# Kernel optimization log

Measured on AMD Instinct MI355X. Metric: run time of the kernel, lower is better.

Reference implementation:

```python
import jax, jax.numpy as jnp
import numpy as np

NB, NA, NC, NH, NW = 64, 5, 20, 64, 64
MAX_BBOX = 50
ANCHORS = jnp.array([[1.3221, 1.73145], [3.19275, 4.00944], [5.05587, 8.09892],
                     [9.47112, 4.84053], [11.2364, 10.0071]], dtype=jnp.float32)
COORD_SCALE = 1.0
NOOBJ_SCALE = 1.0
OBJ_SCALE = 1.0
CLASS_SCALE = 1.0
SIL_THRESH = 0.6


def iou_xywh(b1, b2):
    # center-format IoU, matching marvis bbox_ious(x1y1x2y2=False)
    x1, y1, w1, h1 = b1[..., 0], b1[..., 1], b1[..., 2], b1[..., 3]
    x2, y2, w2, h2 = b2[..., 0], b2[..., 1], b2[..., 2], b2[..., 3]
    Mx = jnp.maximum(x1 + w1 * 0.5, x2 + w2 * 0.5)
    mx = jnp.minimum(x1 - w1 * 0.5, x2 - w2 * 0.5)
    My = jnp.maximum(y1 + h1 * 0.5, y2 + h2 * 0.5)
    my = jnp.minimum(y1 - h1 * 0.5, y2 - h2 * 0.5)
    cw = w1 + w2 - (Mx - mx)
    ch = h1 + h2 - (My - my)
    carea = jnp.where((cw <= 0) | (ch <= 0), 0.0, cw * ch)
    uarea = w1 * h1 + w2 * h2 - carea
    return carea / uarea


def setup_inputs():
    key = jax.random.key(0)
    ko, kc, kx, ky, kw, kh = jax.random.split(key, 6)
    output = jax.random.normal(ko, (NB, NA * (5 + NC), NH, NW), dtype=jnp.float32) * 0.5
    cls = jax.random.randint(kc, (NB, MAX_BBOX), 0, NC).astype(jnp.float32)
    bx = jax.random.uniform(kx, (NB, MAX_BBOX), minval=0.05, maxval=0.95)
    by = jax.random.uniform(ky, (NB, MAX_BBOX), minval=0.05, maxval=0.95)
    bw = jax.random.uniform(kw, (NB, MAX_BBOX), minval=0.02, maxval=0.30)
    bh = jax.random.uniform(kh, (NB, MAX_BBOX), minval=0.02, maxval=0.30)
    target = jnp.stack([cls, bx, by, bw, bh], axis=-1).reshape(NB, MAX_BBOX * 5)
    return {"output": output, "target": target}


def _forward(output, target):
    nB, nH, nW = output.shape[0], output.shape[2], output.shape[3]
    nA, nC = NA, NC
    nTot = nB * nA * nH * nW
    out = output.reshape(nB, nA, 5 + nC, nH, nW)
    x = jax.nn.sigmoid(out[:, :, 0])
    y = jax.nn.sigmoid(out[:, :, 1])
    w = jnp.exp(out[:, :, 2])
    h = jnp.exp(out[:, :, 3])
    conf = jax.nn.sigmoid(out[:, :, 4])
    # class logits laid out exactly as torch: [nB*nA*nH*nW, nC]
    cls_logits = out[:, :, 5:].reshape(nB * nA, nC, nH * nW).transpose(0, 2, 1).reshape(nTot, nC)

    grid_x = jnp.arange(nW, dtype=jnp.float32)
    grid_y = jnp.arange(nH, dtype=jnp.float32)
    pred = jnp.stack([
        x + grid_x[None, None, None, :],
        y + grid_y[None, None, :, None],
        w * ANCHORS[None, :, 0, None, None],
        h * ANCHORS[None, :, 1, None, None],
    ], axis=-1)  # [nB, nA, nH, nW, 4] in grid units
    pred = jax.lax.stop_gradient(pred)  # torch builds pred_boxes from .data

    # ---------------- build_targets, vectorized ----------------
    tgt = target.reshape(nB, MAX_BBOX, 5)
    # loop breaks at first x==0 -> prefix validity
    valid = jnp.cumprod((tgt[:, :, 1] != 0).astype(jnp.int32), axis=1).astype(bool)
    scale = jnp.array([nW, nH, nW, nH], dtype=jnp.float32)
    gt = tgt[:, :, 1:5] * scale  # [nB, 50, 4] (gx, gy, gw, gh)

    # part 1: silence conf_mask where any gt IoU > sil_thresh
    ious = iou_xywh(gt[:, :, None, None, None, :], pred[:, None])  # [nB,50,nA,nH,nW]
    ious = jnp.where(valid[:, :, None, None, None], ious, 0.0)
    conf_mask = jnp.where(ious.max(axis=1) > SIL_THRESH, 0.0, NOOBJ_SCALE)  # [nB,nA,nH,nW]

    # part 2: best anchor per gt box (shape-only IoU at origin; anchor_step==2)
    gt0 = jnp.concatenate([jnp.zeros_like(gt[:, :, :2]), gt[:, :, 2:]], axis=-1)
    anc0 = jnp.concatenate([jnp.zeros_like(ANCHORS), ANCHORS], axis=-1)  # [nA,4]
    a_iou = iou_xywh(anc0[None, None], gt0[:, :, None, :])  # [nB,50,nA]
    best_n = jnp.argmax(a_iou, axis=-1)  # first max, matching strict > in torch loop
    gi = gt[:, :, 0].astype(jnp.int32)
    gj = gt[:, :, 1].astype(jnp.int32)
    b_idx = jnp.broadcast_to(jnp.arange(nB)[:, None], (nB, MAX_BBOX))
    flat = ((b_idx * nA + best_n) * nH + gj) * nW + gi  # [nB,50]
    flat_s = jnp.where(valid, flat, nTot).ravel()  # invalid boxes -> dummy slot

    def scatter(base_flat, vals):
        padded = jnp.concatenate([base_flat, jnp.zeros((1,), base_flat.dtype)])
        return padded.at[flat_s].set(vals.ravel())[:nTot]

    zeros_f = jnp.zeros((nTot,), jnp.float32)
    ones_bt = jnp.ones((nB, MAX_BBOX), jnp.float32)
    coord_mask = scatter(zeros_f, ones_bt)
    conf_mask = scatter(conf_mask.ravel(), jnp.full((nB, MAX_BBOX), OBJ_SCALE, jnp.float32))
    cls_mask = scatter(zeros_f, ones_bt)
    tx = scatter(zeros_f, gt[:, :, 0] - gi.astype(jnp.float32))
    ty = scatter(zeros_f, gt[:, :, 1] - gj.astype(jnp.float32))
    tw = scatter(zeros_f, gt[:, :, 2] / ANCHORS[best_n, 0])
    th = scatter(zeros_f, gt[:, :, 3] / ANCHORS[best_n, 1])
    pb = pred.reshape(nTot, 4)[flat]  # gather pred box at assigned cell, [nB,50,4]
    tconf = scatter(zeros_f, iou_xywh(gt, pb))
    tcls = scatter(zeros_f, tgt[:, :, 0])

    shape4 = (nB, nA, nH, nW)
    coord_mask = coord_mask.reshape(shape4)
    conf_mask = jnp.sqrt(conf_mask.reshape(shape4))  # marvis: conf_mask.sqrt()
    tx, ty = tx.reshape(shape4), ty.reshape(shape4)
    tw, th = tw.reshape(shape4), th.reshape(shape4)
    tconf = tconf.reshape(shape4)

    # ---------------- losses ----------------
    loss_x = COORD_SCALE * 0.5 * jnp.sum(((x - tx) * coord_mask) ** 2)
    loss_y = COORD_SCALE * 0.5 * jnp.sum(((y - ty) * coord_mask) ** 2)
    loss_w = COORD_SCALE * 0.5 * jnp.sum(((w - tw) * coord_mask) ** 2)
    loss_h = COORD_SCALE * 0.5 * jnp.sum(((h - th) * coord_mask) ** 2)
    loss_conf = 0.5 * jnp.sum(((conf - tconf) * conf_mask) ** 2)
    logp = jax.nn.log_softmax(cls_logits, axis=-1)  # [nTot, nC]
    labels = tcls.astype(jnp.int32)
    ce = -jnp.take_along_axis(logp, labels[:, None], axis=1)[:, 0]
    loss_cls = CLASS_SCALE * jnp.sum(ce * cls_mask)
    return loss_x + loss_y + loss_w + loss_h + loss_conf + loss_cls


def reference(output, target):
    return _forward(output, target)
```

## Files before the change

kernel.cpp:

```cpp
#include <hip/hip_runtime.h>
#include <cstddef>

#define NB 64
#define NA 5
#define NC 20
#define NH 64
#define NW 64
#define MAXB 50
#define HWSZ (NH * NW)
#define NABLK 64
#define NBBLK 1280
#define NPART (NABLK + NBBLK)

__constant__ float c_aw[NA] = {1.3221f, 3.19275f, 5.05587f, 9.47112f, 11.2364f};
__constant__ float c_ah[NA] = {1.73145f, 4.00944f, 8.09892f, 4.84053f, 10.0071f};

__device__ __forceinline__ float sigmoidf_(float v) {
    return 1.f / (1.f + __expf(-v));
}

__global__ __launch_bounds__(256, 4) void region_loss_main(const float* __restrict__ out,
                                                           const float* __restrict__ tgt,
                                                           float* __restrict__ partials) {
    const int bid = blockIdx.x;
    const int t = threadIdx.x;

    __shared__ __align__(16) float sbox[MAXB][8];
    __shared__ float s_cls[MAXB], s_gx[MAXB], s_gy[MAXB], s_gw[MAXB], s_gh[MAXB];
    __shared__ int s_flat[MAXB], s_bestn[MAXB];
    __shared__ int s_nv;
    __shared__ float sred[4];

    if (bid < NABLK) {
        const int b = bid;
        if (t < 64) {
            float xv = (t < MAXB) ? tgt[(size_t)b * (MAXB * 5) + t * 5 + 1] : 0.f;
            unsigned long long mk = __ballot(xv != 0.f);
            unsigned long long inv = (~mk) & ((1ull << MAXB) - 1ull);
            int nv_ = inv ? (__ffsll(inv) - 1) : MAXB;
            if (t == 0) s_nv = nv_;
            if (t < MAXB) {
                bool val = t < nv_;
                const float* tp = tgt + (size_t)b * (MAXB * 5) + t * 5;
                float gx = tp[1] * (float)NW, gy = tp[2] * (float)NH;
                float gw = tp[3] * (float)NW, gh = tp[4] * (float)NH;
                s_cls[t] = tp[0];
                s_gx[t] = gx; s_gy[t] = gy; s_gw[t] = gw; s_gh[t] = gh;
                sbox[t][0] = val ? gx - 0.5f * gw : 0.f;
                sbox[t][1] = val ? gx + 0.5f * gw : 0.f;
                sbox[t][2] = val ? gy - 0.5f * gh : 0.f;
                sbox[t][3] = val ? gy + 0.5f * gh : 0.f;
                sbox[t][4] = val ? 0.375f * gw * gh : 1e30f;
            }
        }
        __syncthreads();
        const int nv = s_nv;

        if (t < MAXB) {
            if (t < nv) {
                float gw = s_gw[t], gh = s_gh[t];
                float best = -1.f; int bn = 0;
#pragma unroll
                for (int a = 0; a < NA; ++a) {
                    float ca = fminf(c_aw[a], gw) * fminf(c_ah[a], gh);
                    float ua = c_aw[a] * c_ah[a] + gw * gh - ca;
                    float iou = ca / ua;
                    if (iou > best) { best = iou; bn = a; }
                }
                int gi = (int)s_gx[t], gj = (int)s_gy[t];
                s_bestn[t] = bn;
                s_flat[t] = (bn * NH + gj) * NW + gi;
            } else {
                s_flat[t] = -1 - t;
            }
        }
        __syncthreads();

        float loss = 0.f;
        if (t < nv) {
            bool winner = true;
            const int myf = s_flat[t];
#pragma unroll 10
            for (int t2 = 0; t2 < MAXB; ++t2)
                winner &= (t2 <= t) | (s_flat[t2] != myf);
            if (winner) {
                const int a = s_bestn[t];
                const int gi = myf & (NW - 1);
                const int gj = (myf >> 6) & (NH - 1);
                const size_t base = (((size_t)b * NA + a) * 25) * HWSZ + gj * NW + gi;
                float x = sigmoidf_(out[base]);
                float y = sigmoidf_(out[base + HWSZ]);
                float w = __expf(out[base + 2 * HWSZ]);
                float h = __expf(out[base + 3 * HWSZ]);
                float conf = sigmoidf_(out[base + 4 * HWSZ]);

                float gx = s_gx[t], gy = s_gy[t], gw = s_gw[t], gh = s_gh[t];
                float tx = gx - (float)gi, ty = gy - (float)gj;
                float tw = gw / c_aw[a], th = gh / c_ah[a];
                float dx = x - tx, dy = y - ty, dw = w - tw, dh = h - th;
                loss += 0.5f * (dx * dx + dy * dy + dw * dw + dh * dh);

                float px = x + (float)gi, py = y + (float)gj;
                float pw = w * c_aw[a], ph = h * c_ah[a];
                float pxlo = px - 0.5f * pw, pxhi = px + 0.5f * pw;
                float pylo = py - 0.5f * ph, pyhi = py + 0.5f * ph;
                float parea = pw * ph;

                {
                    float cw  = fminf(pxhi, gx + 0.5f * gw) - fmaxf(pxlo, gx - 0.5f * gw);
                    float chh = fminf(pyhi, gy + 0.5f * gh) - fmaxf(pylo, gy - 0.5f * gh);
                    float ca  = fmaxf(cw, 0.f) * fmaxf(chh, 0.f);
                    float ua  = parea + gw * gh - ca;
                    float tconf = ca / ua;
                    float mm = -1e30f;
#pragma unroll 10
                    for (int t2 = 0; t2 < MAXB; ++t2) {
                        const float4 bb = *reinterpret_cast<const float4*>(&sbox[t2][0]);
                        const float s2 = sbox[t2][4];
                        float cw2 = fminf(pxhi, bb.y) - fmaxf(pxlo, bb.x);
                        float ch2 = fminf(pyhi, bb.w) - fmaxf(pylo, bb.z);
                        mm = fmaxf(mm, fmaf(fmaxf(cw2, 0.f), fmaxf(ch2, 0.f), -s2));
                    }
                    bool sil = mm > 0.375f * parea;
                    float base_c = sil ? 0.f : 0.5f * conf * conf;
                    float dc = conf - tconf;
                    loss += 0.5f * dc * dc - base_c;
                }

                {
                    const int lab = (int)s_cls[t];
                    float mmax = -1e30f, llab = 0.f;
#pragma unroll
                    for (int c = 0; c < NC; ++c) {
                        float l = out[base + (size_t)(5 + c) * HWSZ];
                        mmax = fmaxf(mmax, l);
                        if (c == lab) llab = l;
                    }
                    float se = 0.f;
#pragma unroll
                    for (int c = 0; c < NC; ++c)
                        se += __expf(out[base + (size_t)(5 + c) * HWSZ] - mmax);
                    loss += -(llab - mmax - logf(se));
                }
            }
        }
        if (t < 64) {
            for (int off = 32; off; off >>= 1) loss += __shfl_down(loss, off, 64);
            if (t == 0) partials[bid] = loss;
        }
        return;
    }

    const int g = bid - NABLK;
    const int b = g / 20;
    const int ba = g >> 2;
    const int a = ba - b * NA;
    const int hw = ((g & 3) << 10) + (t << 2);
    const int jrow = hw >> 6;

    if (t < 64) {
        float xv = (t < MAXB) ? tgt[(size_t)b * (MAXB * 5) + t * 5 + 1] : 0.f;
        unsigned long long mk = __ballot(xv != 0.f);
        unsigned long long inv = (~mk) & ((1ull << MAXB) - 1ull);
        int nv = inv ? (__ffsll(inv) - 1) : MAXB;
        if (t < MAXB) {
            bool val = t < nv;
            const float* tp = tgt + (size_t)b * (MAXB * 5) + t * 5;
            float gx = tp[1] * (float)NW, gy = tp[2] * (float)NH;
            float gw = tp[3] * (float)NW, gh = tp[4] * (float)NH;
            sbox[t][0] = val ? gx - 0.5f * gw : 0.f;
            sbox[t][1] = val ? gx + 0.5f * gw : 0.f;
            sbox[t][2] = val ? gy - 0.5f * gh : 0.f;
            sbox[t][3] = val ? gy + 0.5f * gh : 0.f;
            sbox[t][4] = val ? 0.375f * gw * gh : 1e30f;
            sbox[t][5] = gy;
            sbox[t][6] = val ? gh : -1e9f;
            sbox[t][7] = val ? gw * gh : 0.f;
        }
    }

    const float* p = out + (size_t)ba * (25 * HWSZ) + hw;
    const float4 vx = *reinterpret_cast<const float4*>(p);
    const float4 vy = *reinterpret_cast<const float4*>(p + HWSZ);
    const float4 vw = *reinterpret_cast<const float4*>(p + 2 * HWSZ);
    const float4 vh = *reinterpret_cast<const float4*>(p + 3 * HWSZ);
    const float4 vc = *reinterpret_cast<const float4*>(p + 4 * HWSZ);

    const float aw = c_aw[a], ah = c_ah[a];
    const float fj = (float)jrow;
    const float fi0 = (float)(hw & 63);

    float pxlo[4], pxhi[4], pylo[4], pyhi[4], m4[4], rhs[4], hc[4];
    {
        const float xs[4] = {vx.x, vx.y, vx.z, vx.w};
        const float ys[4] = {vy.x, vy.y, vy.z, vy.w};
        const float ws[4] = {vw.x, vw.y, vw.z, vw.w};
        const float hs[4] = {vh.x, vh.y, vh.z, vh.w};
        const float cs[4] = {vc.x, vc.y, vc.z, vc.w};
#pragma unroll
        for (int k = 0; k < 4; ++k) {
            float px = sigmoidf_(xs[k]) + fi0 + (float)k;
            float py = sigmoidf_(ys[k]) + fj;
            float pw = __expf(ws[k]) * aw;
            float ph = __expf(hs[k]) * ah;
            float cf = sigmoidf_(cs[k]);
            pxlo[k] = px - 0.5f * pw; pxhi[k] = px + 0.5f * pw;
            pylo[k] = py - 0.5f * ph; pyhi[k] = py + 0.5f * ph;
            rhs[k] = 0.375f * pw * ph;
            hc[k]  = 0.5f * cf * cf;
            m4[k]  = -1e30f;
        }
    }
    __syncthreads();

    const int lane = t & 63;
    const int li = (lane < MAXB) ? lane : 0;
    const float ls_gy = sbox[li][5];
    const float ls_thr = fmaf(0.7334f, sbox[li][6], 2.01f);
    const float ls_ga = sbox[li][7];
    const float A = aw * ah;
    const float midj = (float)(((g & 3) << 4) + ((t >> 6) << 2)) + 2.0f;
    bool keep = (lane < MAXB) &&
                (fabsf(midj - ls_gy) < ls_thr) &&
                (A >= 0.0505f * ls_ga) && (A <= 19.8f * ls_ga);
    unsigned long long u = __ballot(keep);

    if (u) {
        float4 A0, A1, A2; float S0, S1, S2;
        int n_ = 1;
        { int i0 = __ffsll(u) - 1; u &= u - 1;
          A0 = *reinterpret_cast<const float4*>(&sbox[i0][0]); S0 = sbox[i0][4]; }
        A1 = A0; S1 = S0; A2 = A0; S2 = S0;
        if (u) { int i1 = __ffsll(u) - 1; u &= u - 1;
          A1 = *reinterpret_cast<const float4*>(&sbox[i1][0]); S1 = sbox[i1][4]; ++n_; }
        if (u) { int i2 = __ffsll(u) - 1; u &= u - 1;
          A2 = *reinterpret_cast<const float4*>(&sbox[i2][0]); S2 = sbox[i2][4]; ++n_; }
        for (;;) {
#pragma unroll
            for (int k = 0; k < 4; ++k) {
                float cw = fminf(pxhi[k], A0.y) - fmaxf(pxlo[k], A0.x);
                float ch = fminf(pyhi[k], A0.w) - fmaxf(pylo[k], A0.z);
                m4[k] = fmaxf(m4[k], fmaf(fmaxf(cw, 0.f), fmaxf(ch, 0.f), -S0));
            }
            if (--n_ == 0) break;
            A0 = A1; S0 = S1;
            A1 = A2; S1 = S2;
            if (u) { int in2 = __ffsll(u) - 1; u &= u - 1;
              A2 = *reinterpret_cast<const float4*>(&sbox[in2][0]); S2 = sbox[in2][4]; ++n_; }
        }
    }

    float v = 0.f;
#pragma unroll
    for (int k = 0; k < 4; ++k) v += (m4[k] > rhs[k]) ? 0.f : hc[k];

    for (int off = 32; off; off >>= 1) v += __shfl_down(v, off, 64);
    if ((t & 63) == 0) sred[t >> 6] = v;
    __syncthreads();
    if (t == 0) partials[bid] = sred[0] + sred[1] + sred[2] + sred[3];
}

__global__ __launch_bounds__(256) void reduce_kernel(const float* __restrict__ partials,
                                                     float* __restrict__ outp) {
    float v = 0.f;
    for (int idx = threadIdx.x; idx < NPART; idx += 256) v += partials[idx];
    for (int off = 32; off; off >>= 1) v += __shfl_down(v, off, 64);
    __shared__ float s[4];
    if ((threadIdx.x & 63) == 0) s[threadIdx.x >> 6] = v;
    __syncthreads();
    if (threadIdx.x == 0) outp[0] = s[0] + s[1] + s[2] + s[3];
}

extern "C" void kernel_launch(void* const* d_in, const int* in_sizes, int n_in,
                              void* d_out, int out_size, void* d_ws, size_t ws_size,
                              hipStream_t stream) {
    const float* out_t = (const float*)d_in[0];
    const float* tgt   = (const float*)d_in[1];
    float* loss = (float*)d_out;
    float* partials = (float*)d_ws;

    region_loss_main<<<NPART, 256, 0, stream>>>(out_t, tgt, partials);
    reduce_kernel<<<1, 256, 0, stream>>>(partials, loss);
}
```

Baseline: 25.96 us.

## Fuse reduction via atomics and double per-thread cells with halved grid

Removes the separate reduce kernel. Each block now atomically adds its partial into the output, which is zeroed with a memset beforehand. Each thread processes 8 cells instead of 4, halving the number of no-object blocks, and the row-band culling threshold is widened to match the larger tile. The sigmoid uses a hardware reciprocal and the 3-deep prefetch pipeline in the box loop becomes a simple loop. Float atomics make the summation order nondeterministic, and wider bands may keep more boxes per wave.

```diff
diff --git a/kernel.cpp b/kernel.cpp
--- a/kernel.cpp
+++ b/kernel.cpp
@@ -9,29 +9,30 @@
 #define MAXB 50
 #define HWSZ (NH * NW)
 #define NABLK 64
-#define NBBLK 1280
-#define NPART (NABLK + NBBLK)
+#define NBBLK 640
+#define NGRID (NABLK + NBBLK)
 
 __constant__ float c_aw[NA] = {1.3221f, 3.19275f, 5.05587f, 9.47112f, 11.2364f};
 __constant__ float c_ah[NA] = {1.73145f, 4.00944f, 8.09892f, 4.84053f, 10.0071f};
 
-__device__ __forceinline__ float sigmoidf_(float v) {
-    return 1.f / (1.f + __expf(-v));
+__device__ __forceinline__ float sigmoid_fast(float v) {
+    return __builtin_amdgcn_rcpf(1.f + __expf(-v));
 }
 
-__global__ __launch_bounds__(256, 4) void region_loss_main(const float* __restrict__ out,
-                                                           const float* __restrict__ tgt,
-                                                           float* __restrict__ partials) {
+__global__ __launch_bounds__(256) void region_loss_fused(const float* __restrict__ out,
+                                                         const float* __restrict__ tgt,
+                                                         float* __restrict__ outp) {
     const int bid = blockIdx.x;
     const int t = threadIdx.x;
 
     __shared__ __align__(16) float sbox[MAXB][8];
-    __shared__ float s_cls[MAXB], s_gx[MAXB], s_gy[MAXB], s_gw[MAXB], s_gh[MAXB];
-    __shared__ int s_flat[MAXB], s_bestn[MAXB];
-    __shared__ int s_nv;
     __shared__ float sred[4];
 
     if (bid < NABLK) {
+        __shared__ float s_cls[MAXB], s_gx[MAXB], s_gy[MAXB], s_gw[MAXB], s_gh[MAXB];
+        __shared__ int s_flat[MAXB], s_bestn[MAXB];
+        __shared__ int s_nv;
+
         const int b = bid;
         if (t < 64) {
             float xv = (t < MAXB) ? tgt[(size_t)b * (MAXB * 5) + t * 5 + 1] : 0.f;
@@ -88,11 +89,11 @@
                 const int gi = myf & (NW - 1);
                 const int gj = (myf >> 6) & (NH - 1);
                 const size_t base = (((size_t)b * NA + a) * 25) * HWSZ + gj * NW + gi;
-                float x = sigmoidf_(out[base]);
-                float y = sigmoidf_(out[base + HWSZ]);
+                float x = 1.f / (1.f + __expf(-out[base]));
+                float y = 1.f / (1.f + __expf(-out[base + HWSZ]));
                 float w = __expf(out[base + 2 * HWSZ]);
                 float h = __expf(out[base + 3 * HWSZ]);
-                float conf = sigmoidf_(out[base + 4 * HWSZ]);
+                float conf = 1.f / (1.f + __expf(-out[base + 4 * HWSZ]));
 
                 float gx = s_gx[t], gy = s_gy[t], gw = s_gw[t], gh = s_gh[t];
                 float tx = gx - (float)gi, ty = gy - (float)gj;
@@ -146,16 +147,16 @@
         }
         if (t < 64) {
             for (int off = 32; off; off >>= 1) loss += __shfl_down(loss, off, 64);
-            if (t == 0) partials[bid] = loss;
+            if (t == 0) atomicAdd(outp, loss);
         }
         return;
     }
 
     const int g = bid - NABLK;
-    const int b = g / 20;
-    const int ba = g >> 2;
+    const int ba = g >> 1;
+    const int b = ba / NA;
     const int a = ba - b * NA;
-    const int hw = ((g & 3) << 10) + (t << 2);
+    const int hw = ((g & 1) << 11) + (t << 3);
     const int jrow = hw >> 6;
 
     if (t < 64) {
@@ -180,95 +181,70 @@
     }
 
     const float* p = out + (size_t)ba * (25 * HWSZ) + hw;
-    const float4 vx = *reinterpret_cast<const float4*>(p);
-    const float4 vy = *reinterpret_cast<const float4*>(p + HWSZ);
-    const float4 vw = *reinterpret_cast<const float4*>(p + 2 * HWSZ);
-    const float4 vh = *reinterpret_cast<const float4*>(p + 3 * HWSZ);
-    const float4 vc = *reinterpret_cast<const float4*>(p + 4 * HWSZ);
+    float4 v0[5], v1[5];
+#pragma unroll
+    for (int c = 0; c < 5; ++c) {
+        v0[c] = *reinterpret_cast<const float4*>(p + c * HWSZ);
+        v1[c] = *reinterpret_cast<const float4*>(p + c * HWSZ + 4);
+    }
 
     const float aw = c_aw[a], ah = c_ah[a];
     const float fj = (float)jrow;
     const float fi0 = (float)(hw & 63);
 
-    float pxlo[4], pxhi[4], pylo[4], pyhi[4], m4[4], rhs[4], hc[4];
-    {
-        const float xs[4] = {vx.x, vx.y, vx.z, vx.w};
-        const float ys[4] = {vy.x, vy.y, vy.z, vy.w};
-        const float ws[4] = {vw.x, vw.y, vw.z, vw.w};
-        const float hs[4] = {vh.x, vh.y, vh.z, vh.w};
-        const float cs[4] = {vc.x, vc.y, vc.z, vc.w};
-#pragma unroll
-        for (int k = 0; k < 4; ++k) {
-            float px = sigmoidf_(xs[k]) + fi0 + (float)k;
-            float py = sigmoidf_(ys[k]) + fj;
-            float pw = __expf(ws[k]) * aw;
-            float ph = __expf(hs[k]) * ah;
-            float cf = sigmoidf_(cs[k]);
-            pxlo[k] = px - 0.5f * pw; pxhi[k] = px + 0.5f * pw;
-            pylo[k] = py - 0.5f * ph; pyhi[k] = py + 0.5f * ph;
-            rhs[k] = 0.375f * pw * ph;
-            hc[k]  = 0.5f * cf * cf;
-            m4[k]  = -1e30f;
-        }
+    float pxlo[8], pxhi[8], pylo[8], pyhi[8], m4[8], rhs[8], hc[8];
+#pragma unroll
+    for (int k = 0; k < 8; ++k) {
+        const float4* src = (k < 4) ? v0 : v1;
+        const int kk = k & 3;
+        float xs = (&src[0].x)[kk], ys = (&src[1].x)[kk];
+        float ws = (&src[2].x)[kk], hs = (&src[3].x)[kk], cs = (&src[4].x)[kk];
+        float px = sigmoid_fast(xs) + fi0 + (float)k;
+        float py = sigmoid_fast(ys) + fj;
+        float pw = __expf(ws) * aw;
+        float ph = __expf(hs) * ah;
+        float cf = sigmoid_fast(cs);
+        pxlo[k] = px - 0.5f * pw; pxhi[k] = px + 0.5f * pw;
+        pylo[k] = py - 0.5f * ph; pyhi[k] = py + 0.5f * ph;
+        rhs[k] = 0.375f * pw * ph;
+        hc[k]  = 0.5f * cf * cf;
+        m4[k]  = -1e30f;
     }
     __syncthreads();
 
     const int lane = t & 63;
     const int li = (lane < MAXB) ? lane : 0;
     const float ls_gy = sbox[li][5];
-    const float ls_thr = fmaf(0.7334f, sbox[li][6], 2.01f);
+    const float ls_thr = fmaf(0.7334f, sbox[li][6], 4.01f);
     const float ls_ga = sbox[li][7];
     const float A = aw * ah;
-    const float midj = (float)(((g & 3) << 4) + ((t >> 6) << 2)) + 2.0f;
+    const float midj = (float)(((g & 1) << 5) + ((t >> 6) << 3)) + 4.0f;
     bool keep = (lane < MAXB) &&
                 (fabsf(midj - ls_gy) < ls_thr) &&
                 (A >= 0.0505f * ls_ga) && (A <= 19.8f * ls_ga);
     unsigned long long u = __ballot(keep);
 
-    if (u) {
-        float4 A0, A1, A2; float S0, S1, S2;
-        int n_ = 1;
-        { int i0 = __ffsll(u) - 1; u &= u - 1;
-          A0 = *reinterpret_cast<const float4*>(&sbox[i0][0]); S0 = sbox[i0][4]; }
-        A1 = A0; S1 = S0; A2 = A0; S2 = S0;
-        if (u) { int i1 = __ffsll(u) - 1; u &= u - 1;
-          A1 = *reinterpret_cast<const float4*>(&sbox[i1][0]); S1 = sbox[i1][4]; ++n_; }
-        if (u) { int i2 = __ffsll(u) - 1; u &= u - 1;
-          A2 = *reinterpret_cast<const float4*>(&sbox[i2][0]); S2 = sbox[i2][4]; ++n_; }
-        for (;;) {
-#pragma unroll
-            for (int k = 0; k < 4; ++k) {
-                float cw = fminf(pxhi[k], A0.y) - fmaxf(pxlo[k], A0.x);
-                float ch = fminf(pyhi[k], A0.w) - fmaxf(pylo[k], A0.z);
-                m4[k] = fmaxf(m4[k], fmaf(fmaxf(cw, 0.f), fmaxf(ch, 0.f), -S0));
-            }
-            if (--n_ == 0) break;
-            A0 = A1; S0 = S1;
-            A1 = A2; S1 = S2;
-            if (u) { int in2 = __ffsll(u) - 1; u &= u - 1;
-              A2 = *reinterpret_cast<const float4*>(&sbox[in2][0]); S2 = sbox[in2][4]; ++n_; }
+    while (u) {
+        const int bx = __ffsll(u) - 1;
+        u &= u - 1;
+        const float4 bb = *reinterpret_cast<const float4*>(&sbox[bx][0]);
+        const float s2 = sbox[bx][4];
+#pragma unroll
+        for (int k = 0; k < 8; ++k) {
+            float cw = fminf(pxhi[k], bb.y) - fmaxf(pxlo[k], bb.x);
+            float ch = fminf(pyhi[k], bb.w) - fmaxf(pylo[k], bb.z);
+            m4[k] = fmaxf(m4[k], fmaf(fmaxf(cw, 0.f), fmaxf(ch, 0.f), -s2));
         }
     }
 
     float v = 0.f;
 #pragma unroll
-    for (int k = 0; k < 4; ++k) v += (m4[k] > rhs[k]) ? 0.f : hc[k];
+    for (int k = 0; k < 8; ++k) v += (m4[k] > rhs[k]) ? 0.f : hc[k];
 
     for (int off = 32; off; off >>= 1) v += __shfl_down(v, off, 64);
     if ((t & 63) == 0) sred[t >> 6] = v;
     __syncthreads();
-    if (t == 0) partials[bid] = sred[0] + sred[1] + sred[2] + sred[3];
-}
-
-__global__ __launch_bounds__(256) void reduce_kernel(const float* __restrict__ partials,
-                                                     float* __restrict__ outp) {
-    float v = 0.f;
-    for (int idx = threadIdx.x; idx < NPART; idx += 256) v += partials[idx];
-    for (int off = 32; off; off >>= 1) v += __shfl_down(v, off, 64);
-    __shared__ float s[4];
-    if ((threadIdx.x & 63) == 0) s[threadIdx.x >> 6] = v;
-    __syncthreads();
-    if (threadIdx.x == 0) outp[0] = s[0] + s[1] + s[2] + s[3];
+    if (t == 0) atomicAdd(outp, sred[0] + sred[1] + sred[2] + sred[3]);
 }
 
 extern "C" void kernel_launch(void* const* d_in, const int* in_sizes, int n_in,
@@ -277,8 +253,7 @@
     const float* out_t = (const float*)d_in[0];
     const float* tgt   = (const float*)d_in[1];
     float* loss = (float*)d_out;
-    float* partials = (float*)d_ws;
-
-    region_loss_main<<<NPART, 256, 0, stream>>>(out_t, tgt, partials);
-    reduce_kernel<<<1, 256, 0, stream>>>(partials, loss);
+
+    hipMemsetAsync(loss, 0, sizeof(float), stream);
+    region_loss_fused<<<NGRID, 256, 0, stream>>>(out_t, tgt, loss);
 }
```

Measured after the change: 28.79 us. 1.11x slower.
